# Optimization experiments

Measured on AMD Instinct MI355X. Metric: run time of the kernel, lower is better.

Reference implementation:

```python
import jax, jax.numpy as jnp
import numpy as np

NUM_HEADS = 12

def setup_inputs() -> dict:
    key = jax.random.key(0)
    ks = jax.random.split(key, 9)
    B, N, C = 4, 1024, 768
    hd = C // NUM_HEADS  # 64
    return {
        "x": jax.random.normal(ks[0], (B, N, C), dtype=jnp.float32),
        "prev_attn": jax.random.uniform(ks[1], (B, NUM_HEADS, N, N), dtype=jnp.float32) / N,
        "qkv_w": jax.random.normal(ks[2], (3 * C, C), dtype=jnp.float32) * 0.02,
        "proj_w": jax.random.normal(ks[3], (C, C), dtype=jnp.float32) * 0.02,
        "proj_b": jax.random.normal(ks[4], (C,), dtype=jnp.float32) * 0.02,
        "bp_w1": jax.random.normal(ks[5], (hd // 2, 2 * hd), dtype=jnp.float32) * 0.02,
        "bp_b1": jax.random.normal(ks[6], (hd // 2,), dtype=jnp.float32) * 0.02,
        "bp_w2": jax.random.normal(ks[7], (3, hd // 2), dtype=jnp.float32) * 0.02,
        "bp_b2": jax.random.normal(ks[8], (3,), dtype=jnp.float32) * 0.02,
    }

def reference(x, prev_attn, qkv_w, proj_w, proj_b, bp_w1, bp_b1, bp_w2, bp_b2):
    B, N, C = x.shape
    H = NUM_HEADS
    hd = C // H
    scale = hd ** -0.5
    # qkv projection: [B,N,3C] -> [3,B,H,N,hd]
    qkv = (x @ qkv_w.T).reshape(B, N, 3, H, hd).transpose(2, 0, 3, 1, 4)
    q, k, v = qkv[0], qkv[1], qkv[2]
    # scaled dot-product scores [B,H,N,N]
    attn_logits = jnp.einsum('bhnd,bhmd->bhnm', q, k) * scale
    cur_attn = jax.nn.softmax(attn_logits, axis=-1)
    # per-(b,h,n) bias MLP on concat(q,k): [B,H,N,2*hd] -> [B,H,N,3]
    qk = jnp.concatenate((q, k), axis=-1)
    h1 = jax.nn.relu(jnp.einsum('bhnd,od->bhno', qk, bp_w1) + bp_b1)
    bias = jnp.abs(jnp.einsum('bhno,po->bhnp', h1, bp_w2) + bp_b2)  # [B,H,N,3]
    # blend current attention, previous attention, and uniform term
    attn = (cur_attn * (1.0 + bias[..., 0:1])
            + prev_attn * bias[..., 1:2]
            - bias[..., 2:3] / N)
    out = jnp.einsum('bhnm,bhmd->bhnd', attn, v)  # [B,H,N,hd]
    out = out.transpose(0, 2, 1, 3).reshape(B, N, C)
    out = out @ proj_w.T + proj_b
    return (out, cur_attn)
```

## Files before the change

### kernel.cpp

```cpp
#include <hip/hip_runtime.h>

typedef __bf16 bf16_t;
typedef __bf16 bf16x8 __attribute__((ext_vector_type(8)));
typedef __bf16 bf16x4 __attribute__((ext_vector_type(4)));
typedef float f32x4 __attribute__((ext_vector_type(4)));

static constexpr int Bb = 4, Hh = 12, Nn = 1024, Cc = 768, HD = 64;
static constexpr int OUT0 = Bb * Nn * Cc;

#define GLD16(gp, lp)                                                       \
  __builtin_amdgcn_global_load_lds(                                         \
      (const __attribute__((address_space(1))) unsigned int*)(gp),          \
      (__attribute__((address_space(3))) unsigned int*)(lp), 16, 0, 0)

__global__ __launch_bounds__(256) void convert_all(
    const float* __restrict__ x, const float* __restrict__ qw, const float* __restrict__ pw,
    bf16_t* __restrict__ xb, bf16_t* __restrict__ qwb, bf16_t* __restrict__ pwb) {
  const int NX = (Bb * Nn * Cc) / 4;
  const int NQ = (3 * Cc * Cc) / 4;
  int i = blockIdx.x * 256 + threadIdx.x;
  const float4* src;
  bf16_t* dst;
  int off;
  if (i < NX) { src = (const float4*)x; dst = xb; off = i; }
  else if (i < NX + NQ) { src = (const float4*)qw; dst = qwb; off = i - NX; }
  else { src = (const float4*)pw; dst = pwb; off = i - NX - NQ; }
  float4 v = src[off];
  bf16x4 o;
  o[0] = (bf16_t)v.x; o[1] = (bf16_t)v.y; o[2] = (bf16_t)v.z; o[3] = (bf16_t)v.w;
  *(bf16x4*)(dst + (size_t)off * 4) = o;
}

__global__ __launch_bounds__(256) void gemm_qkv(
    const bf16_t* __restrict__ A, const bf16_t* __restrict__ Bm,
    bf16_t* __restrict__ q_bf, bf16_t* __restrict__ k_bf, bf16_t* __restrict__ vT_bf) {
  __shared__ bf16_t As[128 * 32];
  __shared__ bf16_t Bs[128 * 32];
  const int tid = threadIdx.x;
  const int lane = tid & 63;
  const int w = tid >> 6;
  const int wr = w >> 1, wc = w & 1;
  const int g = lane >> 4, r = lane & 15;
  const int m0 = (blockIdx.x / 18) << 7;
  const int n0 = (blockIdx.x % 18) << 7;

  const f32x4 fz = {0.f, 0.f, 0.f, 0.f};
  f32x4 acc[4][4];
#pragma unroll
  for (int i = 0; i < 4; i++)
#pragma unroll
    for (int j = 0; j < 4; j++) acc[i][j] = fz;

  for (int k0 = 0; k0 < 768; k0 += 32) {
#pragma unroll
    for (int c = 0; c < 2; c++) {
      int row = w * 32 + c * 16 + (lane >> 2);
      int kof = (lane & 3) << 3;
      GLD16(&A[(size_t)(m0 + row) * 768 + k0 + kof], (char*)As + w * 2048 + c * 1024);
      GLD16(&Bm[(size_t)(n0 + row) * 768 + k0 + kof], (char*)Bs + w * 2048 + c * 1024);
    }
    __syncthreads();
    bf16x8 af[4], bfv[4];
#pragma unroll
    for (int i = 0; i < 4; i++) af[i] = *(const bf16x8*)&As[(wr * 64 + i * 16 + r) * 32 + g * 8];
#pragma unroll
    for (int j = 0; j < 4; j++) bfv[j] = *(const bf16x8*)&Bs[(wc * 64 + j * 16 + r) * 32 + g * 8];
#pragma unroll
    for (int i = 0; i < 4; i++)
#pragma unroll
      for (int j = 0; j < 4; j++)
        acc[i][j] = __builtin_amdgcn_mfma_f32_16x16x32_bf16(af[i], bfv[j], acc[i][j], 0, 0, 0);
    __syncthreads();
  }

#pragma unroll
  for (int i = 0; i < 4; i++) {
#pragma unroll
    for (int j = 0; j < 4; j++) {
      int c = n0 + wc * 64 + j * 16 + r;
#pragma unroll
      for (int e = 0; e < 4; e++) {
        int mrow = m0 + wr * 64 + i * 16 + g * 4 + e;
        float val = acc[i][j][e];
        int which = c / 768;
        int cc = c - which * 768;
        int h = cc >> 6, d = cc & 63;
        int b = mrow >> 10, n = mrow & 1023;
        size_t bh = (size_t)(b * Hh + h);
        if (which == 0)      q_bf[(bh * Nn + n) * HD + d] = (bf16_t)val;
        else if (which == 1) k_bf[(bh * Nn + n) * HD + d] = (bf16_t)val;
        else                 vT_bf[(bh * HD + d) * Nn + n] = (bf16_t)val;
      }
    }
  }
}

template <int MODE>
__global__ __launch_bounds__(256) void gemm_bt(
    const bf16_t* __restrict__ A, const bf16_t* __restrict__ Bm, int N, int K,
    float* __restrict__ outF, const float* __restrict__ bias) {
  __shared__ bf16_t As[128 * 40];
  __shared__ bf16_t Bs[128 * 40];
  const int tid = threadIdx.x;
  const int lane = tid & 63;
  const int w = tid >> 6;
  const int wr = w >> 1, wc = w & 1;
  const int g = lane >> 4, r = lane & 15;
  const int ntiles = N >> 7;
  const int m0 = (blockIdx.x / ntiles) << 7;
  const int n0 = (blockIdx.x % ntiles) << 7;

  const f32x4 fz = {0.f, 0.f, 0.f, 0.f};
  f32x4 acc[4][4];
#pragma unroll
  for (int i = 0; i < 4; i++)
#pragma unroll
    for (int j = 0; j < 4; j++) acc[i][j] = fz;

  for (int k0 = 0; k0 < K; k0 += 32) {
#pragma unroll
    for (int p = 0; p < 2; p++) {
      int idx = tid + (p << 8);
      int row = idx >> 2;
      int kof = (idx & 3) << 3;
      *(bf16x8*)&As[row * 40 + kof] = *(const bf16x8*)&A[(size_t)(m0 + row) * K + k0 + kof];
      *(bf16x8*)&Bs[row * 40 + kof] = *(const bf16x8*)&Bm[(size_t)(n0 + row) * K + k0 + kof];
    }
    __syncthreads();
    bf16x8 af[4], bfv[4];
#pragma unroll
    for (int i = 0; i < 4; i++) af[i] = *(const bf16x8*)&As[(wr * 64 + i * 16 + r) * 40 + g * 8];
#pragma unroll
    for (int j = 0; j < 4; j++) bfv[j] = *(const bf16x8*)&Bs[(wc * 64 + j * 16 + r) * 40 + g * 8];
#pragma unroll
    for (int i = 0; i < 4; i++)
#pragma unroll
      for (int j = 0; j < 4; j++)
        acc[i][j] = __builtin_amdgcn_mfma_f32_16x16x32_bf16(af[i], bfv[j], acc[i][j], 0, 0, 0);
    __syncthreads();
  }

#pragma unroll
  for (int i = 0; i < 4; i++) {
#pragma unroll
    for (int j = 0; j < 4; j++) {
      int c = n0 + wc * 64 + j * 16 + r;
#pragma unroll
      for (int e = 0; e < 4; e++) {
        int mrow = m0 + wr * 64 + i * 16 + g * 4 + e;
        outF[(size_t)mrow * N + c] = acc[i][j][e] + bias[c];
      }
    }
  }
}

__global__ __launch_bounds__(256) void bias_mlp(
    const bf16_t* __restrict__ qb, const bf16_t* __restrict__ kb,
    const float* __restrict__ w1, const float* __restrict__ b1,
    const float* __restrict__ w2, const float* __restrict__ b2,
    float* __restrict__ bias4) {
  __shared__ float w1s[32 * 129];
  __shared__ float qks[8][128];
  __shared__ float h1s[8][32];
  const int t = threadIdx.x;
#pragma unroll
  for (int p = 0; p < 16; p++) {
    int idx = p * 256 + t;
    w1s[(idx >> 7) * 129 + (idx & 127)] = w1[idx];
  }
  const int rl = t >> 5, u = t & 31;
  const int rowg = blockIdx.x * 8 + rl;
  {
    int i4 = u * 4;
    const bf16_t* src = (i4 < 64) ? (qb + (size_t)rowg * HD + i4)
                                  : (kb + (size_t)rowg * HD + (i4 - 64));
    bf16x4 vv = *(const bf16x4*)src;
#pragma unroll
    for (int z = 0; z < 4; z++) qks[rl][i4 + z] = (float)vv[z];
  }
  __syncthreads();
  float accv = b1[u];
#pragma unroll 8
  for (int i = 0; i < 128; i++) accv += qks[rl][i] * w1s[u * 129 + i];
  h1s[rl][u] = fmaxf(accv, 0.f);
  __syncthreads();
  if (u < 4) {
    float outv = 0.f;
    if (u < 3) {
      float s = b2[u];
#pragma unroll
      for (int j = 0; j < 32; j++) s += w2[u * 32 + j] * h1s[rl][j];
      float v = fabsf(s);
      outv = (u == 0) ? (1.f + v) : ((u == 1) ? v : -v * (1.f / (float)Nn));
    }
    bias4[(size_t)rowg * 4 + u] = outv;
  }
}

__global__ __launch_bounds__(256, 4) void attn_fused(
    const bf16_t* __restrict__ qb, const bf16_t* __restrict__ kb,
    const bf16_t* __restrict__ vT, const float* __restrict__ prev,
    const float* __restrict__ bias4, float* __restrict__ cur,
    bf16_t* __restrict__ oh) {
  __shared__ char Plb[16 * 2048];
  __shared__ float redmax[16][4];
  __shared__ float redsum[16][4];
  const int bid = blockIdx.x;
  const int tile = (bid & 7) * 384 + (bid >> 3);
  const int bh = tile >> 6, mt = tile & 63;
  const int tid = threadIdx.x;
  const int lane = tid & 63, w = tid >> 6;
  const int g = lane >> 4, r = lane & 15;
  const int row0 = mt << 4;

  const bf16_t* qp = qb + ((size_t)bh * Nn + row0) * HD;
  const bf16_t* kp = kb + (size_t)bh * Nn * HD;
  bf16x8 a0 = *(const bf16x8*)&qp[r * HD + g * 8];
  bf16x8 a1 = *(const bf16x8*)&qp[r * HD + g * 8 + 32];
  const f32x4 fz = {0.f, 0.f, 0.f, 0.f};
  f32x4 acc[16];
#pragma unroll
  for (int t = 0; t < 16; t++) {
    int col = (w << 8) + (t << 4) + r;
    bf16x8 b0 = *(const bf16x8*)&kp[(size_t)col * HD + g * 8];
    bf16x8 b1 = *(const bf16x8*)&kp[(size_t)col * HD + g * 8 + 32];
    f32x4 z = __builtin_amdgcn_mfma_f32_16x16x32_bf16(a0, b0, fz, 0, 0, 0);
    acc[t] = __builtin_amdgcn_mfma_f32_16x16x32_bf16(a1, b1, z, 0, 0, 0);
  }
  const float scale = 0.125f;
  float mj[4] = {-3.0e38f, -3.0e38f, -3.0e38f, -3.0e38f};
#pragma unroll
  for (int t = 0; t < 16; t++)
#pragma unroll
    for (int e = 0; e < 4; e++) {
      acc[t][e] *= scale;
      mj[e] = fmaxf(mj[e], acc[t][e]);
    }
#pragma unroll
  for (int s = 1; s < 16; s <<= 1)
#pragma unroll
    for (int e = 0; e < 4; e++) mj[e] = fmaxf(mj[e], __shfl_xor(mj[e], s, 64));
  if (r == 0) {
#pragma unroll
    for (int e = 0; e < 4; e++) redmax[g * 4 + e][w] = mj[e];
  }
  __syncthreads();
  float rm[4];
#pragma unroll
  for (int e = 0; e < 4; e++) {
    float v = fmaxf(redmax[g * 4 + e][0], redmax[g * 4 + e][1]);
    rm[e] = fmaxf(v, fmaxf(redmax[g * 4 + e][2], redmax[g * 4 + e][3]));
  }
  float sj[4] = {0.f, 0.f, 0.f, 0.f};
#pragma unroll
  for (int t = 0; t < 16; t++)
#pragma unroll
    for (int e = 0; e < 4; e++) {
      float ev = __expf(acc[t][e] - rm[e]);
      acc[t][e] = ev;
      sj[e] += ev;
    }
#pragma unroll
  for (int s = 1; s < 16; s <<= 1)
#pragma unroll
    for (int e = 0; e < 4; e++) sj[e] += __shfl_xor(sj[e], s, 64);
  if (r == 0) {
#pragma unroll
    for (int e = 0; e < 4; e++) redsum[g * 4 + e][w] = sj[e];
  }
  __syncthreads();
  float inv[4];
#pragma unroll
  for (int e = 0; e < 4; e++)
    inv[e] = 1.f / (redsum[g * 4 + e][0] + redsum[g * 4 + e][1] +
                    redsum[g * 4 + e][2] + redsum[g * 4 + e][3]);
#pragma unroll
  for (int t = 0; t < 16; t++) {
    int col = (w << 8) + (t << 4) + r;
#pragma unroll
    for (int e = 0; e < 4; e++) {
      int row = g * 4 + e;
      int off = (row * 2048 + col * 2) ^ ((row & 7) << 4);
      *(bf16_t*)(Plb + off) = (bf16_t)(acc[t][e] * inv[e]);
    }
  }
  __syncthreads();

  const int c4 = tid << 2;
  const float* pp = prev + (size_t)bh * Nn * Nn + (size_t)row0 * Nn + c4;
  float* cp = cur + (size_t)bh * Nn * Nn + (size_t)row0 * Nn + c4;
  const float* bp = bias4 + ((size_t)(bh << 10) + row0) * 4;
#pragma unroll
  for (int half = 0; half < 2; half++) {
    float4 pv[8];
#pragma unroll
    for (int i = 0; i < 8; i++)
      pv[i] = *(const float4*)&pp[(size_t)(half * 8 + i) * Nn];
#pragma unroll
    for (int i = 0; i < 8; i++) {
      int row = half * 8 + i;
      int off = (row * 2048 + c4 * 2) ^ ((row & 7) << 4);
      bf16x4 p4 = *(const bf16x4*)(Plb + off);
      float4 pf;
      pf.x = (float)p4[0]; pf.y = (float)p4[1]; pf.z = (float)p4[2]; pf.w = (float)p4[3];
      *(float4*)&cp[(size_t)row * Nn] = pf;
      float4 bv = *(const float4*)&bp[row * 4];
      bf16x4 nb;
      nb[0] = (bf16_t)(bv.x * pf.x + bv.y * pv[i].x + bv.z);
      nb[1] = (bf16_t)(bv.x * pf.y + bv.y * pv[i].y + bv.z);
      nb[2] = (bf16_t)(bv.x * pf.z + bv.y * pv[i].z + bv.z);
      nb[3] = (bf16_t)(bv.x * pf.w + bv.y * pv[i].w + bv.z);
      *(bf16x4*)(Plb + off) = nb;
    }
  }
  __syncthreads();

  const bf16_t* vrow = vT + (size_t)bh * HD * Nn + (size_t)((w << 4) + r) * Nn;
  f32x4 c0 = fz, c1 = fz, c2 = fz, c3 = fz;
#pragma unroll
  for (int ks = 0; ks < 8; ks++) {
    int kA = ks << 5;
    bf16x8 pA = *(const bf16x8*)(Plb + ((r * 2048 + (kA + g * 8) * 2) ^ ((r & 7) << 4)));
    bf16x8 pB = *(const bf16x8*)(Plb + ((r * 2048 + (256 + kA + g * 8) * 2) ^ ((r & 7) << 4)));
    bf16x8 pC = *(const bf16x8*)(Plb + ((r * 2048 + (512 + kA + g * 8) * 2) ^ ((r & 7) << 4)));
    bf16x8 pD = *(const bf16x8*)(Plb + ((r * 2048 + (768 + kA + g * 8) * 2) ^ ((r & 7) << 4)));
    bf16x8 vA = *(const bf16x8*)&vrow[kA + g * 8];
    bf16x8 vB = *(const bf16x8*)&vrow[256 + kA + g * 8];
    bf16x8 vC = *(const bf16x8*)&vrow[512 + kA + g * 8];
    bf16x8 vD = *(const bf16x8*)&vrow[768 + kA + g * 8];
    c0 = __builtin_amdgcn_mfma_f32_16x16x32_bf16(pA, vA, c0, 0, 0, 0);
    c1 = __builtin_amdgcn_mfma_f32_16x16x32_bf16(pB, vB, c1, 0, 0, 0);
    c2 = __builtin_amdgcn_mfma_f32_16x16x32_bf16(pC, vC, c2, 0, 0, 0);
    c3 = __builtin_amdgcn_mfma_f32_16x16x32_bf16(pD, vD, c3, 0, 0, 0);
  }
  f32x4 osum = (c0 + c1) + (c2 + c3);
  const int b = bh / Hh, h = bh % Hh;
#pragma unroll
  for (int e = 0; e < 4; e++) {
    int nrow = row0 + g * 4 + e;
    oh[((size_t)(b * Nn + nrow)) * Cc + h * HD + (w << 4) + r] = (bf16_t)osum[e];
  }
}

extern "C" void kernel_launch(void* const* d_in, const int* in_sizes, int n_in,
                              void* d_out, int out_size, void* d_ws, size_t ws_size,
                              hipStream_t stream) {
  const float* x      = (const float*)d_in[0];
  const float* prev   = (const float*)d_in[1];
  const float* qkv_w  = (const float*)d_in[2];
  const float* proj_w = (const float*)d_in[3];
  const float* proj_b = (const float*)d_in[4];
  const float* bp_w1  = (const float*)d_in[5];
  const float* bp_b1  = (const float*)d_in[6];
  const float* bp_w2  = (const float*)d_in[7];
  const float* bp_w2b = (const float*)d_in[8];

  float* out0 = (float*)d_out;
  float* cur  = out0 + OUT0;

  char* ws = (char*)d_ws;
  bf16_t* xb    = (bf16_t*)(ws + 0);
  bf16_t* qwb   = (bf16_t*)(ws + 6291456);
  bf16_t* pwb   = (bf16_t*)(ws + 9830400);
  bf16_t* qbf   = (bf16_t*)(ws + 11010048);
  bf16_t* kbf   = (bf16_t*)(ws + 17301504);
  bf16_t* vtb   = (bf16_t*)(ws + 23592960);
  float*  bias4 = (float*)(ws + 29884416);
  bf16_t* ohb   = (bf16_t*)(ws + 30670848);
  if (ws_size < 36962304) return;

  convert_all<<<5376, 256, 0, stream>>>(x, qkv_w, proj_w, xb, qwb, pwb);
  gemm_qkv<<<32 * 18, 256, 0, stream>>>(xb, qwb, qbf, kbf, vtb);
  bias_mlp<<<49152 / 8, 256, 0, stream>>>(qbf, kbf, bp_w1, bp_b1, bp_w2, bp_w2b, bias4);
  attn_fused<<<3072, 256, 0, stream>>>(qbf, kbf, vtb, prev, bias4, cur, ohb);
  gemm_bt<1><<<(4096 / 128) * (768 / 128), 256, 0, stream>>>(
      ohb, pwb, 768, 768, out0, proj_b);
}
```

Baseline: 240.9 us.

## Swap MFMA operands so softmax rows live per-lane and fuse prev/cur epilogue

The QK^T MFMA now takes K as the A operand and Q as B, so each lane holds four consecutive columns of one row. That lets the softmax reduce mostly in registers and write cur_attn and the blended bf16 P straight from registers, dropping one LDS round-trip and a barrier. The 1/8 scale is folded into Q before the bf16 MFMA. prev_attn is prefetched right after the QK matmul to overlap its global load with softmax work. Occupancy hint drops from 4 to 3 blocks per SM to make room for the extra registers, and the bias MLP pads its LDS rows to 130 floats and uses float2 reads. Folding the scale into bf16 Q adds rounding error, and holding prefetched prev values in registers raises register pressure.

New measurement: 247.3 us. 2.6% more time.

```diff
diff --git a/kernel.cpp b/kernel.cpp
--- a/kernel.cpp
+++ b/kernel.cpp
@@ -159,14 +159,14 @@
     const float* __restrict__ w1, const float* __restrict__ b1,
     const float* __restrict__ w2, const float* __restrict__ b2,
     float* __restrict__ bias4) {
-  __shared__ float w1s[32 * 129];
+  __shared__ float w1s[32 * 130];
   __shared__ float qks[8][128];
   __shared__ float h1s[8][32];
   const int t = threadIdx.x;
 #pragma unroll
   for (int p = 0; p < 16; p++) {
     int idx = p * 256 + t;
-    w1s[(idx >> 7) * 129 + (idx & 127)] = w1[idx];
+    w1s[(idx >> 7) * 130 + (idx & 127)] = w1[idx];
   }
   const int rl = t >> 5, u = t & 31;
   const int rowg = blockIdx.x * 8 + rl;
@@ -180,8 +180,12 @@
   }
   __syncthreads();
   float accv = b1[u];
-#pragma unroll 8
-  for (int i = 0; i < 128; i++) accv += qks[rl][i] * w1s[u * 129 + i];
+#pragma unroll 16
+  for (int i2 = 0; i2 < 64; i2++) {
+    float2 wv = *(const float2*)&w1s[u * 130 + i2 * 2];
+    float2 qv = *(const float2*)&qks[rl][i2 * 2];
+    accv += wv.x * qv.x + wv.y * qv.y;
+  }
   h1s[rl][u] = fmaxf(accv, 0.f);
   __syncthreads();
   if (u < 4) {
@@ -197,7 +201,7 @@
   }
 }
 
-__global__ __launch_bounds__(256, 4) void attn_fused(
+__global__ __launch_bounds__(256, 3) void attn_fused(
     const bf16_t* __restrict__ qb, const bf16_t* __restrict__ kb,
     const bf16_t* __restrict__ vT, const float* __restrict__ prev,
     const float* __restrict__ bias4, float* __restrict__ cur,
@@ -212,106 +216,83 @@
   const int lane = tid & 63, w = tid >> 6;
   const int g = lane >> 4, r = lane & 15;
   const int row0 = mt << 4;
+  const int cbase = w << 8;
 
   const bf16_t* qp = qb + ((size_t)bh * Nn + row0) * HD;
   const bf16_t* kp = kb + (size_t)bh * Nn * HD;
-  bf16x8 a0 = *(const bf16x8*)&qp[r * HD + g * 8];
-  bf16x8 a1 = *(const bf16x8*)&qp[r * HD + g * 8 + 32];
+  bf16x8 qr0 = *(const bf16x8*)&qp[r * HD + g * 8];
+  bf16x8 qr1 = *(const bf16x8*)&qp[r * HD + g * 8 + 32];
+  bf16x8 qa0, qa1;
+#pragma unroll
+  for (int j = 0; j < 8; j++) {
+    qa0[j] = (bf16_t)((float)qr0[j] * 0.125f);
+    qa1[j] = (bf16_t)((float)qr1[j] * 0.125f);
+  }
   const f32x4 fz = {0.f, 0.f, 0.f, 0.f};
   f32x4 acc[16];
 #pragma unroll
   for (int t = 0; t < 16; t++) {
-    int col = (w << 8) + (t << 4) + r;
-    bf16x8 b0 = *(const bf16x8*)&kp[(size_t)col * HD + g * 8];
-    bf16x8 b1 = *(const bf16x8*)&kp[(size_t)col * HD + g * 8 + 32];
-    f32x4 z = __builtin_amdgcn_mfma_f32_16x16x32_bf16(a0, b0, fz, 0, 0, 0);
-    acc[t] = __builtin_amdgcn_mfma_f32_16x16x32_bf16(a1, b1, z, 0, 0, 0);
-  }
-  const float scale = 0.125f;
-  float mj[4] = {-3.0e38f, -3.0e38f, -3.0e38f, -3.0e38f};
+    int col = cbase + (t << 4) + r;
+    bf16x8 kf0 = *(const bf16x8*)&kp[(size_t)col * HD + g * 8];
+    bf16x8 kf1 = *(const bf16x8*)&kp[(size_t)col * HD + g * 8 + 32];
+    f32x4 z = __builtin_amdgcn_mfma_f32_16x16x32_bf16(kf0, qa0, fz, 0, 0, 0);
+    acc[t] = __builtin_amdgcn_mfma_f32_16x16x32_bf16(kf1, qa1, z, 0, 0, 0);
+  }
+
+  const float* ppr = prev + (size_t)bh * Nn * Nn + (size_t)(row0 + r) * Nn + cbase + (g << 2);
+  float4 pv[16];
+#pragma unroll
+  for (int t = 0; t < 16; t++) pv[t] = *(const float4*)&ppr[t << 4];
+
+  float mj = -3.0e38f;
 #pragma unroll
   for (int t = 0; t < 16; t++)
 #pragma unroll
+    for (int e = 0; e < 4; e++) mj = fmaxf(mj, acc[t][e]);
+  mj = fmaxf(mj, __shfl_xor(mj, 16, 64));
+  mj = fmaxf(mj, __shfl_xor(mj, 32, 64));
+  if (lane < 16) redmax[lane][w] = mj;
+  __syncthreads();
+  float rm;
+  {
+    float v0 = fmaxf(redmax[r][0], redmax[r][1]);
+    rm = fmaxf(v0, fmaxf(redmax[r][2], redmax[r][3]));
+  }
+  float sj = 0.f;
+#pragma unroll
+  for (int t = 0; t < 16; t++)
+#pragma unroll
     for (int e = 0; e < 4; e++) {
-      acc[t][e] *= scale;
-      mj[e] = fmaxf(mj[e], acc[t][e]);
-    }
-#pragma unroll
-  for (int s = 1; s < 16; s <<= 1)
-#pragma unroll
-    for (int e = 0; e < 4; e++) mj[e] = fmaxf(mj[e], __shfl_xor(mj[e], s, 64));
-  if (r == 0) {
-#pragma unroll
-    for (int e = 0; e < 4; e++) redmax[g * 4 + e][w] = mj[e];
-  }
-  __syncthreads();
-  float rm[4];
-#pragma unroll
-  for (int e = 0; e < 4; e++) {
-    float v = fmaxf(redmax[g * 4 + e][0], redmax[g * 4 + e][1]);
-    rm[e] = fmaxf(v, fmaxf(redmax[g * 4 + e][2], redmax[g * 4 + e][3]));
-  }
-  float sj[4] = {0.f, 0.f, 0.f, 0.f};
-#pragma unroll
-  for (int t = 0; t < 16; t++)
-#pragma unroll
-    for (int e = 0; e < 4; e++) {
-      float ev = __expf(acc[t][e] - rm[e]);
+      float ev = __expf(acc[t][e] - rm);
       acc[t][e] = ev;
-      sj[e] += ev;
-    }
-#pragma unroll
-  for (int s = 1; s < 16; s <<= 1)
-#pragma unroll
-    for (int e = 0; e < 4; e++) sj[e] += __shfl_xor(sj[e], s, 64);
-  if (r == 0) {
-#pragma unroll
-    for (int e = 0; e < 4; e++) redsum[g * 4 + e][w] = sj[e];
-  }
-  __syncthreads();
-  float inv[4];
-#pragma unroll
-  for (int e = 0; e < 4; e++)
-    inv[e] = 1.f / (redsum[g * 4 + e][0] + redsum[g * 4 + e][1] +
-                    redsum[g * 4 + e][2] + redsum[g * 4 + e][3]);
+      sj += ev;
+    }
+  sj += __shfl_xor(sj, 16, 64);
+  sj += __shfl_xor(sj, 32, 64);
+  if (lane < 16) redsum[lane][w] = sj;
+  __syncthreads();
+  const float inv =
+      1.f / (redsum[r][0] + redsum[r][1] + redsum[r][2] + redsum[r][3]);
+
+  const float4 bvr = *(const float4*)&bias4[((size_t)bh * 1024 + row0 + r) * 4];
+  const float b0c = bvr.x, b1c = bvr.y, b2c = bvr.z;
+  float* cp = cur + (size_t)bh * Nn * Nn + (size_t)(row0 + r) * Nn + cbase + (g << 2);
 #pragma unroll
   for (int t = 0; t < 16; t++) {
-    int col = (w << 8) + (t << 4) + r;
-#pragma unroll
-    for (int e = 0; e < 4; e++) {
-      int row = g * 4 + e;
-      int off = (row * 2048 + col * 2) ^ ((row & 7) << 4);
-      *(bf16_t*)(Plb + off) = (bf16_t)(acc[t][e] * inv[e]);
-    }
-  }
-  __syncthreads();
-
-  const int c4 = tid << 2;
-  const float* pp = prev + (size_t)bh * Nn * Nn + (size_t)row0 * Nn + c4;
-  float* cp = cur + (size_t)bh * Nn * Nn + (size_t)row0 * Nn + c4;
-  const float* bp = bias4 + ((size_t)(bh << 10) + row0) * 4;
-#pragma unroll
-  for (int half = 0; half < 2; half++) {
-    float4 pv[8];
-#pragma unroll
-    for (int i = 0; i < 8; i++)
-      pv[i] = *(const float4*)&pp[(size_t)(half * 8 + i) * Nn];
-#pragma unroll
-    for (int i = 0; i < 8; i++) {
-      int row = half * 8 + i;
-      int off = (row * 2048 + c4 * 2) ^ ((row & 7) << 4);
-      bf16x4 p4 = *(const bf16x4*)(Plb + off);
-      float4 pf;
-      pf.x = (float)p4[0]; pf.y = (float)p4[1]; pf.z = (float)p4[2]; pf.w = (float)p4[3];
-      *(float4*)&cp[(size_t)row * Nn] = pf;
-      float4 bv = *(const float4*)&bp[row * 4];
-      bf16x4 nb;
-      nb[0] = (bf16_t)(bv.x * pf.x + bv.y * pv[i].x + bv.z);
-      nb[1] = (bf16_t)(bv.x * pf.y + bv.y * pv[i].y + bv.z);
-      nb[2] = (bf16_t)(bv.x * pf.z + bv.y * pv[i].z + bv.z);
-      nb[3] = (bf16_t)(bv.x * pf.w + bv.y * pv[i].w + bv.z);
-      *(bf16x4*)(Plb + off) = nb;
-    }
+    float4 p;
+    p.x = acc[t][0] * inv;
+    p.y = acc[t][1] * inv;
+    p.z = acc[t][2] * inv;
+    p.w = acc[t][3] * inv;
+    *(float4*)&cp[t << 4] = p;
+    bf16x4 nb;
+    nb[0] = (bf16_t)(b0c * p.x + b1c * pv[t].x + b2c);
+    nb[1] = (bf16_t)(b0c * p.y + b1c * pv[t].y + b2c);
+    nb[2] = (bf16_t)(b0c * p.z + b1c * pv[t].z + b2c);
+    nb[3] = (bf16_t)(b0c * p.w + b1c * pv[t].w + b2c);
+    int col = cbase + (t << 4) + (g << 2);
+    int off = (r * 2048 + col * 2) ^ ((r & 7) << 4);
+    *(bf16x4*)(Plb + off) = nb;
   }
   __syncthreads();
 
```
